# Optimization experiments

Hardware: AMD Instinct MI355X
Metric: run time of the kernel (lower is better)

The kernel has to match this reference:

```python
import jax, jax.numpy as jnp
import numpy as np
import math

INPUT_SIZE = 512
DK = 64
B, N = 8, 2048

def setup_inputs() -> dict:
    key = jax.random.key(0)
    k1, k2, k3, k4, k5, k6 = jax.random.split(key, 6)
    X = jax.random.normal(k1, (B, N, INPUT_SIZE), dtype=jnp.float32)
    h = jax.random.normal(k2, (B, N, INPUT_SIZE), dtype=jnp.float32)
    s = 1.0 / math.sqrt(INPUT_SIZE)
    WQ = jax.random.uniform(k3, (INPUT_SIZE, DK), dtype=jnp.float32, minval=-s, maxval=s)
    bQ = jax.random.uniform(k4, (DK,), dtype=jnp.float32, minval=-s, maxval=s)
    WK = jax.random.uniform(k5, (INPUT_SIZE, DK), dtype=jnp.float32, minval=-s, maxval=s)
    bK = jax.random.uniform(k6, (DK,), dtype=jnp.float32, minval=-s, maxval=s)
    return {"X": X, "h": h, "WQ": WQ, "bQ": bQ, "WK": WK, "bK": bK}

def reference(X, h, WQ, bQ, WK, bK):
    # Q = linearQ(h), K = linearK(X); dropout is eval-mode identity
    Q = jnp.einsum('bnd,dk->bnk', h, WQ) + bQ   # [B, N, dk]
    K = jnp.einsum('bnd,dk->bnk', X, WK) + bK   # [B, N, dk]
    scores = jnp.einsum('bqk,bnk->bqn', Q, K) / jnp.sqrt(jnp.asarray(DK, X.dtype))
    A = jax.nn.softmax(scores, axis=-1)          # [B, N, N]
    out = jnp.einsum('bqn,bnd->bqd', A, X)       # V = X
    return out
```

## Files before the change

kernel.cpp:

```cpp
#include <hip/hip_runtime.h>
#include <hip/hip_bf16.h>

#define B_ 8
#define N_ 2048
#define D_ 512
#define DK_ 64

typedef float f32x4 __attribute__((ext_vector_type(4)));
typedef short bf16x8 __attribute__((ext_vector_type(8)));
typedef unsigned short u16;

__device__ __forceinline__ u16 f2bf(float f) {
  union { float f; unsigned u; } v; v.f = f;
  unsigned r = v.u + 0x7FFFu + ((v.u >> 16) & 1u);
  return (u16)(r >> 16);
}

#define MFMA16(a, b, cacc) __builtin_amdgcn_mfma_f32_16x16x32_bf16((a), (b), (cacc), 0, 0, 0)

#define BARRIER_LGKM() do {                                   \
    asm volatile("s_waitcnt lgkmcnt(0)" ::: "memory");        \
    __builtin_amdgcn_s_barrier();                             \
    asm volatile("" ::: "memory");                            \
  } while (0)


__global__ __launch_bounds__(256) void vt_kernel(const float* __restrict__ X,
                                                 u16* __restrict__ Vf) {
  int bid = blockIdx.x;
  int dt = bid & 7, nt = (bid >> 3) & 31, b = bid >> 8;
  int n0 = nt * 64, d0 = dt * 64;
  __shared__ u16 T[64 * 72];
  int t = threadIdx.x;
  const float* Xb = X + ((size_t)b * N_ + n0) * D_ + d0;
#pragma unroll
  for (int p = 0; p < 4; ++p) {
    int r = p * 16 + (t >> 4);
    int c4 = (t & 15) * 4;
    f32x4 v = *reinterpret_cast<const f32x4*>(Xb + (size_t)r * D_ + c4);
#pragma unroll
    for (int j = 0; j < 4; ++j) T[(c4 + j) * 72 + r] = f2bf(v[j]);
  }
  __syncthreads();
  int w = t >> 6, l = t & 63, g = l >> 4, c = l & 15;
#pragma unroll
  for (int ks = 0; ks < 2; ++ks) {
    bf16x8 v = *reinterpret_cast<const bf16x8*>(&T[(w * 16 + c) * 72 + ks * 32 + 8 * g]);
    *reinterpret_cast<bf16x8*>(
        Vf + (((size_t)(b * 32 + dt * 4 + w) * 32 + nt) * 2 + ks) * 512 + l * 8) = v;
  }
}

__global__ __launch_bounds__(256) void proj_kernel(
    const float* __restrict__ h, const float* __restrict__ X,
    const float* __restrict__ WQ, const float* __restrict__ bQ,
    const float* __restrict__ WK, const float* __restrict__ bK,
    u16* __restrict__ Qf, u16* __restrict__ Kf) {
  int bid = blockIdx.x;
  int b = bid & 7, nt = bid >> 3;
  int n0 = nt * 64;
  int t = threadIdx.x, w = t >> 6, l = t & 63, g = l >> 4, c = l & 15;
  int arow = n0 + w * 16 + c;
  const float* hrow = h + ((size_t)b * N_ + arow) * D_;
  const float* Xrow = X + ((size_t)b * N_ + arow) * D_;
  f32x4 accq[4], acck[4];
#pragma unroll
  for (int cf = 0; cf < 4; ++cf) {
    accq[cf] = (f32x4){0.f, 0.f, 0.f, 0.f};
    acck[cf] = (f32x4){0.f, 0.f, 0.f, 0.f};
  }
  for (int k0 = 0; k0 < D_; k0 += 32) {
    bf16x8 ah, ax;
    {
      f32x4 h0 = *reinterpret_cast<const f32x4*>(hrow + k0 + 8 * g);
      f32x4 h1 = *reinterpret_cast<const f32x4*>(hrow + k0 + 8 * g + 4);
      f32x4 x0 = *reinterpret_cast<const f32x4*>(Xrow + k0 + 8 * g);
      f32x4 x1 = *reinterpret_cast<const f32x4*>(Xrow + k0 + 8 * g + 4);
#pragma unroll
      for (int i = 0; i < 4; ++i) {
        ah[i] = (short)f2bf(h0[i]); ah[i + 4] = (short)f2bf(h1[i]);
        ax[i] = (short)f2bf(x0[i]); ax[i + 4] = (short)f2bf(x1[i]);
      }
    }
#pragma unroll
    for (int cf = 0; cf < 4; ++cf) {
      bf16x8 bq, bk;
#pragma unroll
      for (int i = 0; i < 8; ++i) {
        int kk = k0 + 8 * g + i;
        bq[i] = (short)f2bf(WQ[(size_t)kk * DK_ + cf * 16 + c]);
        bk[i] = (short)f2bf(WK[(size_t)kk * DK_ + cf * 16 + c]);
      }
      accq[cf] = MFMA16(ah, bq, accq[cf]);
      acck[cf] = MFMA16(ax, bk, acck[cf]);
    }
  }
#pragma unroll
  for (int cf = 0; cf < 4; ++cf) {
    float vq = bQ[cf * 16 + c], vk = bK[cf * 16 + c];
    int ks = cf >> 1;
    int g2 = ((cf & 1) * 16 + c) >> 3;
    int i2 = c & 7;
#pragma unroll
    for (int r = 0; r < 4; ++r) {
      size_t e = ((size_t)(b * 128 + nt * 4 + w) * 2 + ks) * 512 +
                 (g2 * 16 + 4 * g + r) * 8 + i2;
      Qf[e] = f2bf((accq[cf][r] + vq) * 0.125f);
      Kf[e] = f2bf(acck[cf][r] + vk);
    }
  }
}

__global__ __launch_bounds__(512, 1) void attn_kernel(
    const u16* __restrict__ Qf, const u16* __restrict__ Kf,
    const u16* __restrict__ Vf, float* __restrict__ out) {
  int bid = blockIdx.x;
  int b = bid & 7, qt = bid >> 3;
  int q0 = qt * 64;
  int t = threadIdx.x, w = t >> 6, l = t & 63, g = l >> 4, c = l & 15;
  int qh = w >> 1, kq = w & 1;

  __shared__ u16 Plds[2][64][40];
  __shared__ float Lp[2][64];

  bf16x8 aq[2];
#pragma unroll
  for (int ks = 0; ks < 2; ++ks)
    aq[ks] = *reinterpret_cast<const bf16x8*>(
        Qf + ((size_t)(b * 128 + qt * 4 + qh) * 2 + ks) * 512 + l * 8);

  f32x4 o[4][4];
#pragma unroll
  for (int a = 0; a < 4; ++a)
#pragma unroll
    for (int d = 0; d < 4; ++d) o[a][d] = (f32x4){0.f, 0.f, 0.f, 0.f};
  float lp[4] = {0.f, 0.f, 0.f, 0.f};

  const u16* Kbase = Kf + ((size_t)(b * 256 + 2 * kq)) * 512 + l * 8;
  const u16* Vbase = Vf + ((size_t)(b * 32 + w * 4) * 64) * 512 + l * 8;

  bf16x8 kbuf[4][2], vbuf[4][4];

#pragma unroll
  for (int j = 0; j < 3; ++j) {
#pragma unroll
    for (int ks = 0; ks < 2; ++ks)
      kbuf[j][ks] = *reinterpret_cast<const bf16x8*>(
          Kbase + (size_t)(4 * j + ks) * 512);
#pragma unroll
    for (int f = 0; f < 4; ++f)
      vbuf[j][f] = *reinterpret_cast<const bf16x8*>(
          Vbase + (size_t)(f * 64 + j) * 512);
  }
  {
    f32x4 s = (f32x4){0.f, 0.f, 0.f, 0.f};
    s = MFMA16(aq[0], kbuf[0][0], s);
    s = MFMA16(aq[1], kbuf[0][1], s);
#pragma unroll
    for (int r = 0; r < 4; ++r) {
      float p = __expf(s[r]); lp[r] += p;
      Plds[0][qh * 16 + 4 * g + r][kq * 16 + c] = f2bf(p);
    }
  }
  BARRIER_LGKM();

  auto body = [&](bf16x8 (&kS)[2], bf16x8 (&kL)[2],
                  bf16x8 (&vR)[4], bf16x8 (&vL)[4], int i) {
    const int kvL = (i + 3) & 63;
    const int pbW = (i + 1) & 1, pbR = i & 1;

#pragma unroll
    for (int ks = 0; ks < 2; ++ks)
      kL[ks] = *reinterpret_cast<const bf16x8*>(
          Kbase + (size_t)(4 * kvL + ks) * 512);
#pragma unroll
    for (int f = 0; f < 4; ++f)
      vL[f] = *reinterpret_cast<const bf16x8*>(
          Vbase + (size_t)(f * 64 + kvL) * 512);

    f32x4 s = (f32x4){0.f, 0.f, 0.f, 0.f};
    s = MFMA16(aq[0], kS[0], s);
    s = MFMA16(aq[1], kS[1], s);

#pragma unroll
    for (int r = 0; r < 4; ++r) {
      float p = __expf(s[r]); lp[r] += p;
      Plds[pbW][qh * 16 + 4 * g + r][kq * 16 + c] = f2bf(p);
    }

    bf16x8 pa0 = *reinterpret_cast<const bf16x8*>(&Plds[pbR][c][8 * g]);
    bf16x8 pa1 = *reinterpret_cast<const bf16x8*>(&Plds[pbR][16 + c][8 * g]);
    bf16x8 pa2 = *reinterpret_cast<const bf16x8*>(&Plds[pbR][32 + c][8 * g]);
    bf16x8 pa3 = *reinterpret_cast<const bf16x8*>(&Plds[pbR][48 + c][8 * g]);
    __builtin_amdgcn_s_setprio(1);
#pragma unroll
    for (int dt = 0; dt < 4; ++dt) {
      o[0][dt] = MFMA16(pa0, vR[dt], o[0][dt]);
      o[1][dt] = MFMA16(pa1, vR[dt], o[1][dt]);
      o[2][dt] = MFMA16(pa2, vR[dt], o[2][dt]);
      o[3][dt] = MFMA16(pa3, vR[dt], o[3][dt]);
    }
    __builtin_amdgcn_s_setprio(0);

    BARRIER_LGKM();
  };

#pragma unroll 1
  for (int i = 0; i < 60; i += 4) {
    body(kbuf[1], kbuf[3], vbuf[0], vbuf[3], i);
    body(kbuf[2], kbuf[0], vbuf[1], vbuf[0], i + 1);
    body(kbuf[3], kbuf[1], vbuf[2], vbuf[1], i + 2);
    body(kbuf[0], kbuf[2], vbuf[3], vbuf[2], i + 3);
  }
  body(kbuf[1], kbuf[3], vbuf[0], vbuf[3], 60);
  body(kbuf[2], kbuf[0], vbuf[1], vbuf[0], 61);
  body(kbuf[3], kbuf[1], vbuf[2], vbuf[1], 62);

  {
    bf16x8 pa0 = *reinterpret_cast<const bf16x8*>(&Plds[1][c][8 * g]);
    bf16x8 pa1 = *reinterpret_cast<const bf16x8*>(&Plds[1][16 + c][8 * g]);
    bf16x8 pa2 = *reinterpret_cast<const bf16x8*>(&Plds[1][32 + c][8 * g]);
    bf16x8 pa3 = *reinterpret_cast<const bf16x8*>(&Plds[1][48 + c][8 * g]);
#pragma unroll
    for (int dt = 0; dt < 4; ++dt) {
      o[0][dt] = MFMA16(pa0, vbuf[3][dt], o[0][dt]);
      o[1][dt] = MFMA16(pa1, vbuf[3][dt], o[1][dt]);
      o[2][dt] = MFMA16(pa2, vbuf[3][dt], o[2][dt]);
      o[3][dt] = MFMA16(pa3, vbuf[3][dt], o[3][dt]);
    }
  }

#pragma unroll
  for (int r = 0; r < 4; ++r) {
    float v = lp[r];
    v += __shfl_xor(v, 1); v += __shfl_xor(v, 2);
    v += __shfl_xor(v, 4); v += __shfl_xor(v, 8);
    lp[r] = v;
  }
  if (c == 0) {
#pragma unroll
    for (int r = 0; r < 4; ++r) Lp[kq][qh * 16 + 4 * g + r] = lp[r];
  }
  __syncthreads();

  float* outb = out + ((size_t)b * N_ + q0) * D_;
#pragma unroll
  for (int qf2 = 0; qf2 < 4; ++qf2)
#pragma unroll
    for (int r = 0; r < 4; ++r) {
      int ql = qf2 * 16 + 4 * g + r;
      float L = Lp[0][ql] + Lp[1][ql];
      float inv = 1.0f / L;
#pragma unroll
      for (int df = 0; df < 4; ++df)
        outb[(size_t)ql * D_ + w * 64 + df * 16 + c] = o[qf2][df][r] * inv;
    }
}

extern "C" void kernel_launch(void* const* d_in, const int* in_sizes, int n_in,
                              void* d_out, int out_size, void* d_ws, size_t ws_size,
                              hipStream_t stream) {
  const float* X  = (const float*)d_in[0];
  const float* h  = (const float*)d_in[1];
  const float* WQ = (const float*)d_in[2];
  const float* bQ = (const float*)d_in[3];
  const float* WK = (const float*)d_in[4];
  const float* bK = (const float*)d_in[5];
  float* out = (float*)d_out;

  u16* Vf = (u16*)d_ws;
  u16* Qf = Vf + (size_t)B_ * D_ * N_;
  u16* Kf = Qf + (size_t)B_ * N_ * DK_;

  vt_kernel<<<dim3(2048), dim3(256), 0, stream>>>(X, Vf);
  proj_kernel<<<dim3(256), dim3(256), 0, stream>>>(h, X, WQ, bQ, WK, bK, Qf, Kf);
  attn_kernel<<<dim3(256), dim3(512), 0, stream>>>(Qf, Kf, Vf, out);
}
```

Before: 80.51 us.

## Halve attention query tile to 32 rows and double grid for occupancy

The attention kernel now processes 32 query rows per block instead of 64 and launches 512 blocks instead of 256. Launch bounds are raised to allow multiple blocks per CU. The score computation is duplicated across two warp groups, with only one group writing P to shared memory. K/V register buffering is reduced from four-deep to two-deep prefetch, and V loads move after the PV MFMAs. This cuts per-thread registers and fills more of the 256 CUs, at the cost of redundant QK^T/exp work and twice the total K/V streaming.

```diff
diff --git a/kernel.cpp b/kernel.cpp
--- a/kernel.cpp
+++ b/kernel.cpp
@@ -111,27 +111,27 @@
   }
 }
 
-__global__ __launch_bounds__(512, 1) void attn_kernel(
+__global__ __launch_bounds__(512, 4) void attn_kernel(
     const u16* __restrict__ Qf, const u16* __restrict__ Kf,
     const u16* __restrict__ Vf, float* __restrict__ out) {
   int bid = blockIdx.x;
   int b = bid & 7, qt = bid >> 3;
-  int q0 = qt * 64;
+  int q0 = qt * 32;
   int t = threadIdx.x, w = t >> 6, l = t & 63, g = l >> 4, c = l & 15;
-  int qh = w >> 1, kq = w & 1;
-
-  __shared__ u16 Plds[2][64][40];
-  __shared__ float Lp[2][64];
+  int qh = w & 1, kq = (w >> 1) & 1, dup = w >> 2;
+
+  __shared__ u16 Plds[2][32][76];
+  __shared__ float Lp[2][32];
 
   bf16x8 aq[2];
 #pragma unroll
   for (int ks = 0; ks < 2; ++ks)
     aq[ks] = *reinterpret_cast<const bf16x8*>(
-        Qf + ((size_t)(b * 128 + qt * 4 + qh) * 2 + ks) * 512 + l * 8);
-
-  f32x4 o[4][4];
-#pragma unroll
-  for (int a = 0; a < 4; ++a)
+        Qf + ((size_t)(b * 128 + qt * 2 + qh) * 2 + ks) * 512 + l * 8);
+
+  f32x4 o[2][4];
+#pragma unroll
+  for (int a = 0; a < 2; ++a)
 #pragma unroll
     for (int d = 0; d < 4; ++d) o[a][d] = (f32x4){0.f, 0.f, 0.f, 0.f};
   float lp[4] = {0.f, 0.f, 0.f, 0.f};
@@ -139,10 +139,10 @@
   const u16* Kbase = Kf + ((size_t)(b * 256 + 2 * kq)) * 512 + l * 8;
   const u16* Vbase = Vf + ((size_t)(b * 32 + w * 4) * 64) * 512 + l * 8;
 
-  bf16x8 kbuf[4][2], vbuf[4][4];
-
-#pragma unroll
-  for (int j = 0; j < 3; ++j) {
+  bf16x8 kbuf[2][2], vbuf[2][4];
+
+#pragma unroll
+  for (int j = 0; j < 2; ++j) {
 #pragma unroll
     for (int ks = 0; ks < 2; ++ks)
       kbuf[j][ks] = *reinterpret_cast<const bf16x8*>(
@@ -159,24 +159,20 @@
 #pragma unroll
     for (int r = 0; r < 4; ++r) {
       float p = __expf(s[r]); lp[r] += p;
-      Plds[0][qh * 16 + 4 * g + r][kq * 16 + c] = f2bf(p);
+      if (dup == 0) Plds[0][qh * 16 + 4 * g + r][kq * 16 + c] = f2bf(p);
     }
   }
   BARRIER_LGKM();
 
-  auto body = [&](bf16x8 (&kS)[2], bf16x8 (&kL)[2],
-                  bf16x8 (&vR)[4], bf16x8 (&vL)[4], int i) {
-    const int kvL = (i + 3) & 63;
+  auto body = [&](bf16x8 (&kFree)[2], bf16x8 (&kS)[2],
+                  bf16x8 (&vCur)[4], int i) {
+    const int jn = (i + 2) & 63;
     const int pbW = (i + 1) & 1, pbR = i & 1;
 
 #pragma unroll
     for (int ks = 0; ks < 2; ++ks)
-      kL[ks] = *reinterpret_cast<const bf16x8*>(
-          Kbase + (size_t)(4 * kvL + ks) * 512);
-#pragma unroll
-    for (int f = 0; f < 4; ++f)
-      vL[f] = *reinterpret_cast<const bf16x8*>(
-          Vbase + (size_t)(f * 64 + kvL) * 512);
+      kFree[ks] = *reinterpret_cast<const bf16x8*>(
+          Kbase + (size_t)(4 * jn + ks) * 512);
 
     f32x4 s = (f32x4){0.f, 0.f, 0.f, 0.f};
     s = MFMA16(aq[0], kS[0], s);
@@ -185,48 +181,41 @@
 #pragma unroll
     for (int r = 0; r < 4; ++r) {
       float p = __expf(s[r]); lp[r] += p;
-      Plds[pbW][qh * 16 + 4 * g + r][kq * 16 + c] = f2bf(p);
+      if (dup == 0) Plds[pbW][qh * 16 + 4 * g + r][kq * 16 + c] = f2bf(p);
     }
 
     bf16x8 pa0 = *reinterpret_cast<const bf16x8*>(&Plds[pbR][c][8 * g]);
     bf16x8 pa1 = *reinterpret_cast<const bf16x8*>(&Plds[pbR][16 + c][8 * g]);
-    bf16x8 pa2 = *reinterpret_cast<const bf16x8*>(&Plds[pbR][32 + c][8 * g]);
-    bf16x8 pa3 = *reinterpret_cast<const bf16x8*>(&Plds[pbR][48 + c][8 * g]);
     __builtin_amdgcn_s_setprio(1);
 #pragma unroll
-    for (int dt = 0; dt < 4; ++dt) {
-      o[0][dt] = MFMA16(pa0, vR[dt], o[0][dt]);
-      o[1][dt] = MFMA16(pa1, vR[dt], o[1][dt]);
-      o[2][dt] = MFMA16(pa2, vR[dt], o[2][dt]);
-      o[3][dt] = MFMA16(pa3, vR[dt], o[3][dt]);
+    for (int df = 0; df < 4; ++df) {
+      o[0][df] = MFMA16(pa0, vCur[df], o[0][df]);
+      o[1][df] = MFMA16(pa1, vCur[df], o[1][df]);
     }
     __builtin_amdgcn_s_setprio(0);
+
+#pragma unroll
+    for (int f = 0; f < 4; ++f)
+      vCur[f] = *reinterpret_cast<const bf16x8*>(
+          Vbase + (size_t)(f * 64 + jn) * 512);
 
     BARRIER_LGKM();
   };
 
 #pragma unroll 1
-  for (int i = 0; i < 60; i += 4) {
-    body(kbuf[1], kbuf[3], vbuf[0], vbuf[3], i);
-    body(kbuf[2], kbuf[0], vbuf[1], vbuf[0], i + 1);
-    body(kbuf[3], kbuf[1], vbuf[2], vbuf[1], i + 2);
-    body(kbuf[0], kbuf[2], vbuf[3], vbuf[2], i + 3);
-  }
-  body(kbuf[1], kbuf[3], vbuf[0], vbuf[3], 60);
-  body(kbuf[2], kbuf[0], vbuf[1], vbuf[0], 61);
-  body(kbuf[3], kbuf[1], vbuf[2], vbuf[1], 62);
+  for (int i = 0; i < 62; i += 2) {
+    body(kbuf[0], kbuf[1], vbuf[0], i);
+    body(kbuf[1], kbuf[0], vbuf[1], i + 1);
+  }
+  body(kbuf[0], kbuf[1], vbuf[0], 62);
 
   {
     bf16x8 pa0 = *reinterpret_cast<const bf16x8*>(&Plds[1][c][8 * g]);
     bf16x8 pa1 = *reinterpret_cast<const bf16x8*>(&Plds[1][16 + c][8 * g]);
-    bf16x8 pa2 = *reinterpret_cast<const bf16x8*>(&Plds[1][32 + c][8 * g]);
-    bf16x8 pa3 = *reinterpret_cast<const bf16x8*>(&Plds[1][48 + c][8 * g]);
-#pragma unroll
-    for (int dt = 0; dt < 4; ++dt) {
-      o[0][dt] = MFMA16(pa0, vbuf[3][dt], o[0][dt]);
-      o[1][dt] = MFMA16(pa1, vbuf[3][dt], o[1][dt]);
-      o[2][dt] = MFMA16(pa2, vbuf[3][dt], o[2][dt]);
-      o[3][dt] = MFMA16(pa3, vbuf[3][dt], o[3][dt]);
+#pragma unroll
+    for (int df = 0; df < 4; ++df) {
+      o[0][df] = MFMA16(pa0, vbuf[1][df], o[0][df]);
+      o[1][df] = MFMA16(pa1, vbuf[1][df], o[1][df]);
     }
   }
 
@@ -237,7 +226,7 @@
     v += __shfl_xor(v, 4); v += __shfl_xor(v, 8);
     lp[r] = v;
   }
-  if (c == 0) {
+  if (dup == 0 && c == 0) {
 #pragma unroll
     for (int r = 0; r < 4; ++r) Lp[kq][qh * 16 + 4 * g + r] = lp[r];
   }
@@ -245,15 +234,15 @@
 
   float* outb = out + ((size_t)b * N_ + q0) * D_;
 #pragma unroll
-  for (int qf2 = 0; qf2 < 4; ++qf2)
-#pragma unroll
-    for (int r = 0; r < 4; ++r) {
-      int ql = qf2 * 16 + 4 * g + r;
+  for (int a = 0; a < 2; ++a)
+#pragma unroll
+    for (int r = 0; r < 4; ++r) {
+      int ql = a * 16 + 4 * g + r;
       float L = Lp[0][ql] + Lp[1][ql];
       float inv = 1.0f / L;
 #pragma unroll
       for (int df = 0; df < 4; ++df)
-        outb[(size_t)ql * D_ + w * 64 + df * 16 + c] = o[qf2][df][r] * inv;
+        outb[(size_t)ql * D_ + w * 64 + df * 16 + c] = o[a][df][r] * inv;
     }
 }
 
@@ -274,5 +263,5 @@
 
   vt_kernel<<<dim3(2048), dim3(256), 0, stream>>>(X, Vf);
   proj_kernel<<<dim3(256), dim3(256), 0, stream>>>(h, X, WQ, bQ, WK, bK, Qf, Kf);
-  attn_kernel<<<dim3(256), dim3(512), 0, stream>>>(Qf, Kf, Vf, out);
-}
+  attn_kernel<<<dim3(512), dim3(512), 0, stream>>>(Qf, Kf, Vf, out);
+}
```

After: 94.33 us. +17.2%, slower.
